# Performance work log

Measured on AMD Instinct MI355X. Metric: run time of the kernel, lower is better.

The kernel has to match this reference:

```python
import jax, jax.numpy as jnp
import numpy as np
import math

B, E, V, D, L = 2, 100000, 12500, 128, 4


def _ln(x, g, b, eps=1e-5):
    m = jnp.mean(x, axis=-1, keepdims=True)
    v = jnp.mean(jnp.square(x - m), axis=-1, keepdims=True)
    return (x - m) / jnp.sqrt(v + eps) * g + b


def setup_inputs() -> dict:
    key = jax.random.key(0)
    ks = jax.random.split(key, 20)
    s = 0.02
    inp = {
        "delta_noisy": jax.random.normal(ks[0], (B, E, 3), jnp.float32),
        "n": jax.random.randint(ks[1], (B,), 0, 1000, jnp.int32),
        "edge_index": jax.random.randint(ks[2], (2, E), 0, V, jnp.int32),
        "num_vertices": V,
        "w_in": jax.random.normal(ks[3], (3, D), jnp.float32) * s,
        "b_in": jnp.zeros((D,), jnp.float32),
        "W1": jax.random.normal(ks[4], (L, 2 * D, D), jnp.float32) * s,
        "b1": jnp.zeros((L, D), jnp.float32),
        "ln_g": jnp.ones((L, D), jnp.float32),
        "ln_b": jnp.zeros((L, D), jnp.float32),
        "W2": jax.random.normal(ks[5], (L, D, D), jnp.float32) * s,
        "b2": jnp.zeros((L, D), jnp.float32),
        "norm_g": jnp.ones((L, D), jnp.float32),
        "norm_b": jnp.zeros((L, D), jnp.float32),
        "te_w1": jax.random.normal(ks[6], (D, 4 * D), jnp.float32) * s,
        "te_b1": jnp.zeros((4 * D,), jnp.float32),
        "te_w2": jax.random.normal(ks[7], (4 * D, D), jnp.float32) * s,
        "te_b2": jnp.zeros((D,), jnp.float32),
        "w_out": jax.random.normal(ks[8], (D, 3), jnp.float32) * s,
        "b_out": jnp.zeros((3,), jnp.float32),
    }
    return inp


def reference(delta_noisy, n, edge_index, num_vertices, w_in, b_in, W1, b1,
              ln_g, ln_b, W2, b2, norm_g, norm_b, te_w1, te_b1, te_w2, te_b2,
              w_out, b_out):
    Bq, Eq, _ = delta_noisy.shape
    Dq = w_in.shape[1]
    src, dst = edge_index[0], edge_index[1]

    # input projection: (B,E,3) -> (B,E,D)
    h = delta_noisy @ w_in + b_in

    # sinusoidal timestep embedding + MLP
    half = Dq // 2
    freqs = jnp.exp(-math.log(10000.0) * jnp.arange(half, dtype=jnp.float32) / half)
    args = n.astype(jnp.float32)[:, None] * freqs[None, :]
    emb = jnp.concatenate([jnp.sin(args), jnp.cos(args)], axis=-1)  # (B,D)
    t_emb = jax.nn.silu(emb @ te_w1 + te_b1) @ te_w2 + te_b2
    h = h + t_emb[:, None, :]

    for i in range(W1.shape[0]):
        # scatter-add edge features into both endpoint vertices: (B,V,D)
        vf = jnp.zeros((Bq, num_vertices, Dq), h.dtype)
        vf = vf.at[:, src].add(h).at[:, dst].add(h)
        # gather back to edges and run edge MLP
        x = jnp.concatenate([vf[:, src, :], vf[:, dst, :]], axis=-1)  # (B,E,2D)
        x = x @ W1[i] + b1[i]
        x = jax.nn.silu(_ln(x, ln_g[i], ln_b[i]))
        x = x @ W2[i] + b2[i]
        h = _ln(h + x, norm_g[i], norm_b[i])

    return h @ w_out + b_out
```

## Files before the change

### kernel.cpp

```cpp
#include <hip/hip_runtime.h>
#include <math.h>

#define Bc 2
#define Ec 100000
#define Vc 12500
#define Dc 128
#define Lc 4

typedef __attribute__((ext_vector_type(4))) float f32x4;
typedef __attribute__((ext_vector_type(8))) short short8s;
typedef __attribute__((ext_vector_type(8))) __bf16 bf16x8;

static __device__ __forceinline__ short f2bf(float f) {
    unsigned u = __builtin_bit_cast(unsigned, f);
    unsigned r = (u + 0x7FFFu + ((u >> 16) & 1u)) >> 16;
    return (short)r;
}

static __device__ __forceinline__ float bf2f(short s) {
    unsigned u = ((unsigned)(unsigned short)s) << 16;
    return __builtin_bit_cast(float, u);
}

static __device__ __forceinline__ f32x4 mfma16(short8s a, short8s b, f32x4 c) {
    return __builtin_amdgcn_mfma_f32_16x16x32_bf16(
        __builtin_bit_cast(bf16x8, a), __builtin_bit_cast(bf16x8, b), c, 0, 0, 0);
}

#define SWZ(row, bytecol) ((((row) * 256) + (bytecol)) ^ (((row) & 7) << 4))

__global__ void t_emb_kernel(const int* __restrict__ n,
                             const float* __restrict__ te_w1, const float* __restrict__ te_b1,
                             const float* __restrict__ te_w2, const float* __restrict__ te_b2,
                             float* __restrict__ t_emb) {
    const int b = blockIdx.x;
    const int t = threadIdx.x;
    __shared__ float emb[Dc];
    __shared__ float hid[4 * Dc];
    const float nf = (float)n[b];
    const int half = Dc / 2;
    {
        int j = (t < half) ? t : (t - half);
        float freq = expf(-logf(10000.0f) * (float)j / (float)half);
        float arg = nf * freq;
        emb[t] = (t < half) ? sinf(arg) : cosf(arg);
    }
    __syncthreads();
    for (int jj = 0; jj < 4; ++jj) {
        int c = t + jj * Dc;
        float acc = te_b1[c];
        for (int k = 0; k < Dc; ++k) acc += emb[k] * te_w1[k * (4 * Dc) + c];
        hid[c] = acc / (1.0f + expf(-acc));
    }
    __syncthreads();
    float acc = te_b2[t];
    for (int k = 0; k < 4 * Dc; ++k) acc += hid[k] * te_w2[k * Dc + t];
    t_emb[b * Dc + t] = acc;
}

__global__ void input_proj_kernel(const float* __restrict__ delta,
                                  const float* __restrict__ w_in, const float* __restrict__ b_in,
                                  const float* __restrict__ t_emb,
                                  unsigned short* __restrict__ h) {
    int idx = blockIdx.x * blockDim.x + threadIdx.x;
    const int total = Bc * Ec * (Dc / 4);
    if (idx >= total) return;
    int dq = idx & (Dc / 4 - 1);
    int be = idx >> 5;
    int b = be / Ec;
    const float* dd = delta + (size_t)be * 3;
    float d0 = dd[0], d1 = dd[1], d2 = dd[2];
    float4 acc = ((const float4*)b_in)[dq];
    float4 te = ((const float4*)t_emb)[b * (Dc / 4) + dq];
    float4 w0 = ((const float4*)w_in)[dq];
    float4 w1 = ((const float4*)w_in)[(Dc / 4) + dq];
    float4 w2 = ((const float4*)w_in)[2 * (Dc / 4) + dq];
    acc.x += te.x + d0 * w0.x + d1 * w1.x + d2 * w2.x;
    acc.y += te.y + d0 * w0.y + d1 * w1.y + d2 * w2.y;
    acc.z += te.z + d0 * w0.z + d1 * w1.z + d2 * w2.z;
    acc.w += te.w + d0 * w0.w + d1 * w1.w + d2 * w2.w;
    short4 p;
    p.x = f2bf(acc.x); p.y = f2bf(acc.y); p.z = f2bf(acc.z); p.w = f2bf(acc.w);
    ((short4*)h)[idx] = p;
}

__global__ void convert_w_kernel(const float* __restrict__ W1, const float* __restrict__ W2,
                                 short* __restrict__ w1f, short* __restrict__ w2f) {
    int idx = blockIdx.x * blockDim.x + threadIdx.x;
    if (idx < Lc * 32768) {
        int l = idx >> 15;
        int j = idx & 7;
        int lane = (idx >> 3) & 63;
        int ks = (idx >> 9) & 7;
        int nt = (idx >> 12) & 7;
        int r = lane & 15, g = lane >> 4;
        int n = nt * 16 + r;
        int k = 32 * ks + 8 * g + j;
        w1f[idx] = f2bf(W1[((size_t)l * 256 + k) * 128 + n]);
    }
    if (idx < Lc * 16384) {
        int l = idx >> 14;
        int j = idx & 7;
        int lane = (idx >> 3) & 63;
        int ks = (idx >> 9) & 3;
        int nt = (idx >> 11) & 7;
        int r = lane & 15, g = lane >> 4;
        int n = nt * 16 + r;
        int k = 32 * ks + 8 * g + j;
        w2f[idx] = f2bf(W2[((size_t)l * 128 + k) * 128 + n]);
    }
}

__global__ void csr_zero_kernel(int* __restrict__ cnt) {
    int i = blockIdx.x * blockDim.x + threadIdx.x;
    if (i < Vc) cnt[i] = 0;
}

__global__ void csr_count_kernel(const int* __restrict__ src, const int* __restrict__ dst,
                                 int* __restrict__ cnt) {
    int i = blockIdx.x * blockDim.x + threadIdx.x;
    if (i >= 2 * Ec) return;
    int v = (i < Ec) ? src[i] : dst[i - Ec];
    atomicAdd(&cnt[v], 1);
}

__global__ void csr_scan_kernel(const int* __restrict__ cnt,
                                int* __restrict__ off, int* __restrict__ cur) {
    __shared__ int part[256];
    const int t = threadIdx.x;
    const int CH = (Vc + 255) / 256;
    int s = 0;
    for (int j = 0; j < CH; ++j) {
        int i = t * CH + j;
        if (i < Vc) s += cnt[i];
    }
    part[t] = s;
    __syncthreads();
    for (int ofs = 1; ofs < 256; ofs <<= 1) {
        int y = (t >= ofs) ? part[t - ofs] : 0;
        __syncthreads();
        part[t] += y;
        __syncthreads();
    }
    int run = part[t] - s;
    for (int j = 0; j < CH; ++j) {
        int i = t * CH + j;
        if (i < Vc) {
            off[i] = run;
            cur[i] = run;
            run += cnt[i];
        }
    }
    if (t == 255) off[Vc] = run;
}

__global__ void csr_fill_kernel(const int* __restrict__ src, const int* __restrict__ dst,
                                int* __restrict__ cur, int* __restrict__ adj) {
    int i = blockIdx.x * blockDim.x + threadIdx.x;
    if (i >= 2 * Ec) return;
    int e = (i < Ec) ? i : (i - Ec);
    int v = (i < Ec) ? src[e] : dst[e];
    int p = atomicAdd(&cur[v], 1);
    adj[p] = e;
}

__global__ void gather_kernel(const unsigned short* __restrict__ h,
                              const int* __restrict__ off, const int* __restrict__ adj,
                              short* __restrict__ vf) {
    int gw = blockIdx.x * 4 + (threadIdx.x >> 6);
    if (gw >= Bc * Vc) return;
    int b = (gw >= Vc) ? 1 : 0;
    int v = gw - b * Vc;
    int lane = threadIdx.x & 63;
    int o0 = off[v], o1 = off[v + 1];
    const short2* hb = (const short2*)(h + (size_t)b * Ec * Dc);
    float ax0 = 0.f, ay0 = 0.f, ax1 = 0.f, ay1 = 0.f;
    float ax2 = 0.f, ay2 = 0.f, ax3 = 0.f, ay3 = 0.f;
    int j = o0;
    for (; j + 4 <= o1; j += 4) {
        int e0 = adj[j], e1 = adj[j + 1], e2 = adj[j + 2], e3 = adj[j + 3];
        short2 x0 = hb[(size_t)e0 * 64 + lane];
        short2 x1 = hb[(size_t)e1 * 64 + lane];
        short2 x2 = hb[(size_t)e2 * 64 + lane];
        short2 x3 = hb[(size_t)e3 * 64 + lane];
        ax0 += bf2f(x0.x); ay0 += bf2f(x0.y);
        ax1 += bf2f(x1.x); ay1 += bf2f(x1.y);
        ax2 += bf2f(x2.x); ay2 += bf2f(x2.y);
        ax3 += bf2f(x3.x); ay3 += bf2f(x3.y);
    }
    for (; j < o1; ++j) {
        int e = adj[j];
        short2 x = hb[(size_t)e * 64 + lane];
        ax0 += bf2f(x.x); ay0 += bf2f(x.y);
    }
    float sx = (ax0 + ax1) + (ax2 + ax3);
    float sy = (ay0 + ay1) + (ay2 + ay3);
    short2 w;
    w.x = f2bf(sx);
    w.y = f2bf(sy);
    ((short2*)vf)[(size_t)gw * (Dc / 2) + lane] = w;
}

__launch_bounds__(64, 3)
__global__ void edge_layer_kernel(unsigned short* __restrict__ h,
                                  const short* __restrict__ vf,
                                  const int* __restrict__ src, const int* __restrict__ dst,
                                  const short* __restrict__ w1f, const float* __restrict__ b1,
                                  const float* __restrict__ ln_g, const float* __restrict__ ln_b,
                                  const short* __restrict__ w2f, const float* __restrict__ b2,
                                  const float* __restrict__ ng, const float* __restrict__ nb,
                                  const float* __restrict__ w_out, const float* __restrict__ b_out,
                                  float* __restrict__ out) {
    __shared__ __align__(16) short x1s[16 * 128];
    char* x1b = (char*)x1s;

    const int lane = threadIdx.x;
    const int r = lane & 15;
    const int g = lane >> 4;
    const int wavebase = blockIdx.x * 32;

    const short *srow[2], *drow[2];
    #pragma unroll
    for (int mt = 0; mt < 2; ++mt) {
        int eg = wavebase + mt * 16 + r;
        int bb = (eg >= Ec) ? 1 : 0;
        int e = eg - bb * Ec;
        srow[mt] = vf + ((size_t)(bb * Vc + src[e])) * Dc;
        drow[mt] = vf + ((size_t)(bb * Vc + dst[e])) * Dc;
    }

    short8s bf[2][8];
    #pragma unroll
    for (int mt = 0; mt < 2; ++mt)
        #pragma unroll
        for (int ks = 0; ks < 4; ++ks) {
            bf[mt][ks]     = *(const short8s*)(srow[mt] + 32 * ks + 8 * g);
            bf[mt][4 + ks] = *(const short8s*)(drow[mt] + 32 * ks + 8 * g);
        }

    f32x4 acc[2][8];
    #pragma unroll
    for (int nt = 0; nt < 8; ++nt) {
        acc[0][nt] = (f32x4){0.f, 0.f, 0.f, 0.f};
        acc[1][nt] = (f32x4){0.f, 0.f, 0.f, 0.f};
        #pragma unroll
        for (int ks = 0; ks < 8; ++ks) {
            short8s afrag = *(const short8s*)(w1f + ((size_t)(nt * 8 + ks) * 64 + lane) * 8);
            acc[0][nt] = mfma16(afrag, bf[0][ks], acc[0][nt]);
            acc[1][nt] = mfma16(afrag, bf[1][ks], acc[1][nt]);
        }
    }

    const bool last = (w_out != nullptr);

    #pragma unroll
    for (int mt = 0; mt < 2; ++mt) {
        const int eg = wavebase + mt * 16 + r;
        unsigned short* hrow = h + (size_t)eg * Dc;

        short4 hpre[8];
        #pragma unroll
        for (int nt = 0; nt < 8; ++nt)
            hpre[nt] = *(const short4*)(hrow + nt * 16 + 4 * g);

        {
            float s = 0.f, ss = 0.f;
            #pragma unroll
            for (int nt = 0; nt < 8; ++nt) {
                const float4 bb = *(const float4*)&b1[nt * 16 + 4 * g];
                acc[mt][nt][0] += bb.x; acc[mt][nt][1] += bb.y;
                acc[mt][nt][2] += bb.z; acc[mt][nt][3] += bb.w;
                #pragma unroll
                for (int i = 0; i < 4; ++i) { float v = acc[mt][nt][i]; s += v; ss += v * v; }
            }
            s += __shfl_xor(s, 16); ss += __shfl_xor(ss, 16);
            s += __shfl_xor(s, 32); ss += __shfl_xor(ss, 32);
            float mean = s * (1.0f / Dc);
            float var = ss * (1.0f / Dc) - mean * mean;
            float rstd = rsqrtf(var + 1e-5f);
            #pragma unroll
            for (int nt = 0; nt < 8; ++nt) {
                const float4 lg = *(const float4*)&ln_g[nt * 16 + 4 * g];
                const float4 lb = *(const float4*)&ln_b[nt * 16 + 4 * g];
                float o[4];
                #pragma unroll
                for (int i = 0; i < 4; ++i) {
                    float gg = (i == 0) ? lg.x : (i == 1) ? lg.y : (i == 2) ? lg.z : lg.w;
                    float bb = (i == 0) ? lb.x : (i == 1) ? lb.y : (i == 2) ? lb.z : lb.w;
                    float xh = (acc[mt][nt][i] - mean) * rstd * gg + bb;
                    o[i] = xh / (1.0f + __expf(-xh));
                }
                short4 st;
                st.x = f2bf(o[0]); st.y = f2bf(o[1]); st.z = f2bf(o[2]); st.w = f2bf(o[3]);
                *(short4*)(x1b + SWZ(r, (nt * 16 + 4 * g) * 2)) = st;
            }
        }

        short8s b2f[4];
        #pragma unroll
        for (int ks = 0; ks < 4; ++ks)
            b2f[ks] = *(const short8s*)(x1b + SWZ(r, (32 * ks + 8 * g) * 2));
        f32x4 acc2[8];
        #pragma unroll
        for (int nt = 0; nt < 8; ++nt) {
            acc2[nt] = (f32x4){0.f, 0.f, 0.f, 0.f};
            #pragma unroll
            for (int ks = 0; ks < 4; ++ks) {
                short8s afrag = *(const short8s*)(w2f + ((size_t)(nt * 4 + ks) * 64 + lane) * 8);
                acc2[nt] = mfma16(afrag, b2f[ks], acc2[nt]);
            }
        }

        float s = 0.f, ss = 0.f;
        #pragma unroll
        for (int nt = 0; nt < 8; ++nt) {
            const float4 bb = *(const float4*)&b2[nt * 16 + 4 * g];
            acc2[nt][0] += bb.x + bf2f(hpre[nt].x);
            acc2[nt][1] += bb.y + bf2f(hpre[nt].y);
            acc2[nt][2] += bb.z + bf2f(hpre[nt].z);
            acc2[nt][3] += bb.w + bf2f(hpre[nt].w);
            #pragma unroll
            for (int i = 0; i < 4; ++i) { float v = acc2[nt][i]; s += v; ss += v * v; }
        }
        s += __shfl_xor(s, 16); ss += __shfl_xor(ss, 16);
        s += __shfl_xor(s, 32); ss += __shfl_xor(ss, 32);
        float mean = s * (1.0f / Dc);
        float var = ss * (1.0f / Dc) - mean * mean;
        float rstd = rsqrtf(var + 1e-5f);
        if (!last) {
            #pragma unroll
            for (int nt = 0; nt < 8; ++nt) {
                const float4 gv = *(const float4*)&ng[nt * 16 + 4 * g];
                const float4 bv = *(const float4*)&nb[nt * 16 + 4 * g];
                short4 o;
                o.x = f2bf((acc2[nt][0] - mean) * rstd * gv.x + bv.x);
                o.y = f2bf((acc2[nt][1] - mean) * rstd * gv.y + bv.y);
                o.z = f2bf((acc2[nt][2] - mean) * rstd * gv.z + bv.z);
                o.w = f2bf((acc2[nt][3] - mean) * rstd * gv.w + bv.w);
                *(short4*)(hrow + nt * 16 + 4 * g) = o;
            }
        } else {
            float a0 = 0.f, a1 = 0.f, a2 = 0.f;
            #pragma unroll
            for (int nt = 0; nt < 8; ++nt) {
                const float4 gv = *(const float4*)&ng[nt * 16 + 4 * g];
                const float4 bv = *(const float4*)&nb[nt * 16 + 4 * g];
                #pragma unroll
                for (int i = 0; i < 4; ++i) {
                    float gg = (i == 0) ? gv.x : (i == 1) ? gv.y : (i == 2) ? gv.z : gv.w;
                    float bb = (i == 0) ? bv.x : (i == 1) ? bv.y : (i == 2) ? bv.z : bv.w;
                    float y = (acc2[nt][i] - mean) * rstd * gg + bb;
                    int nidx = nt * 16 + 4 * g + i;
                    a0 += y * w_out[nidx * 3 + 0];
                    a1 += y * w_out[nidx * 3 + 1];
                    a2 += y * w_out[nidx * 3 + 2];
                }
            }
            a0 += __shfl_xor(a0, 16); a1 += __shfl_xor(a1, 16); a2 += __shfl_xor(a2, 16);
            a0 += __shfl_xor(a0, 32); a1 += __shfl_xor(a1, 32); a2 += __shfl_xor(a2, 32);
            if (g == 0) {
                out[(size_t)eg * 3 + 0] = a0 + b_out[0];
                out[(size_t)eg * 3 + 1] = a1 + b_out[1];
                out[(size_t)eg * 3 + 2] = a2 + b_out[2];
            }
        }
    }
}

extern "C" void kernel_launch(void* const* d_in, const int* in_sizes, int n_in,
                              void* d_out, int out_size, void* d_ws, size_t ws_size,
                              hipStream_t stream) {
    const float* delta = (const float*)d_in[0];
    const int* n = (const int*)d_in[1];
    const int* edge_index = (const int*)d_in[2];
    const float* w_in = (const float*)d_in[4];
    const float* b_in = (const float*)d_in[5];
    const float* W1 = (const float*)d_in[6];
    const float* b1 = (const float*)d_in[7];
    const float* ln_g = (const float*)d_in[8];
    const float* ln_b = (const float*)d_in[9];
    const float* W2 = (const float*)d_in[10];
    const float* b2 = (const float*)d_in[11];
    const float* ng = (const float*)d_in[12];
    const float* nb = (const float*)d_in[13];
    const float* te_w1 = (const float*)d_in[14];
    const float* te_b1 = (const float*)d_in[15];
    const float* te_w2 = (const float*)d_in[16];
    const float* te_b2 = (const float*)d_in[17];
    const float* w_out = (const float*)d_in[18];
    const float* b_out = (const float*)d_in[19];
    float* out = (float*)d_out;

    char* ws = (char*)d_ws;
    size_t o = 0;
    float* t_emb = (float*)(ws + o); o += 1024;
    unsigned short* h = (unsigned short*)(ws + o); o += (size_t)Bc * Ec * Dc * 2;
    short* vf    = (short*)(ws + o); o += (size_t)Bc * Vc * Dc * 2;
    short* w1f   = (short*)(ws + o); o += (size_t)Lc * 32768 * 2;
    short* w2f   = (short*)(ws + o); o += (size_t)Lc * 16384 * 2;
    int* cnt     = (int*)(ws + o);   o += ((size_t)Vc * 4 + 255) / 256 * 256;
    int* off     = (int*)(ws + o);   o += ((size_t)(Vc + 1) * 4 + 255) / 256 * 256;
    int* cur     = (int*)(ws + o);   o += ((size_t)Vc * 4 + 255) / 256 * 256;
    int* adj     = (int*)(ws + o);   o += (size_t)2 * Ec * 4;

    const int* src = edge_index;
    const int* dst = edge_index + Ec;

    t_emb_kernel<<<Bc, Dc, 0, stream>>>(n, te_w1, te_b1, te_w2, te_b2, t_emb);
    convert_w_kernel<<<(Lc * 32768 + 255) / 256, 256, 0, stream>>>(W1, W2, w1f, w2f);

    {
        int total = Bc * Ec * (Dc / 4);
        input_proj_kernel<<<(total + 255) / 256, 256, 0, stream>>>(delta, w_in, b_in, t_emb, h);
    }

    csr_zero_kernel<<<(Vc + 255) / 256, 256, 0, stream>>>(cnt);
    csr_count_kernel<<<(2 * Ec + 255) / 256, 256, 0, stream>>>(src, dst, cnt);
    csr_scan_kernel<<<1, 256, 0, stream>>>(cnt, off, cur);
    csr_fill_kernel<<<(2 * Ec + 255) / 256, 256, 0, stream>>>(src, dst, cur, adj);

    const int eblocks = (Bc * Ec) / 32;
    for (int i = 0; i < Lc; ++i) {
        gather_kernel<<<(Bc * Vc + 3) / 4, 256, 0, stream>>>(h, off, adj, vf);
        edge_layer_kernel<<<eblocks, 64, 0, stream>>>(
            h, vf, src, dst,
            w1f + (size_t)i * 32768, b1 + i * Dc,
            ln_g + i * Dc, ln_b + i * Dc,
            w2f + (size_t)i * 16384, b2 + i * Dc,
            ng + i * Dc, nb + i * Dc,
            (i == Lc - 1) ? w_out : nullptr, b_out, out);
    }
}
```

Measured before the change: 688.2 us.

## Hoist first edge-MLP GEMM to per-vertex projections before gathering to edges

Splits W1 into its src and dst halves and applies each to the vertex features once per vertex in a new vertex_gemm_kernel, writing two bf16 projected tables. The edge kernel then gathers the two projected rows and adds them, skipping the 2D×D GEMM per edge. This cuts first-layer MFMA work by roughly the edge-to-vertex ratio. In exchange it adds a kernel launch, extra workspace and a write/read of two vertex-sized tables, plus an extra bf16 rounding of the projected values before the layer norm.

New measurement: 606.7 us. 1.13x faster.

```diff
diff --git a/kernel.cpp b/kernel.cpp
--- a/kernel.cpp
+++ b/kernel.cpp
@@ -26,8 +26,6 @@
     return __builtin_amdgcn_mfma_f32_16x16x32_bf16(
         __builtin_bit_cast(bf16x8, a), __builtin_bit_cast(bf16x8, b), c, 0, 0, 0);
 }
-
-#define SWZ(row, bytecol) ((((row) * 256) + (bytecol)) ^ (((row) & 7) << 4))
 
 __global__ void t_emb_kernel(const int* __restrict__ n,
                              const float* __restrict__ te_w1, const float* __restrict__ te_b1,
@@ -85,18 +83,19 @@
 }
 
 __global__ void convert_w_kernel(const float* __restrict__ W1, const float* __restrict__ W2,
-                                 short* __restrict__ w1f, short* __restrict__ w2f) {
+                                 short* __restrict__ w1af, short* __restrict__ w2f) {
     int idx = blockIdx.x * blockDim.x + threadIdx.x;
     if (idx < Lc * 32768) {
         int l = idx >> 15;
         int j = idx & 7;
         int lane = (idx >> 3) & 63;
-        int ks = (idx >> 9) & 7;
-        int nt = (idx >> 12) & 7;
+        int ks = (idx >> 9) & 3;
+        int nt = (idx >> 11) & 7;
+        int half = (idx >> 14) & 1;
         int r = lane & 15, g = lane >> 4;
         int n = nt * 16 + r;
-        int k = 32 * ks + 8 * g + j;
-        w1f[idx] = f2bf(W1[((size_t)l * 256 + k) * 128 + n]);
+        int k = half * 128 + 32 * ks + 8 * g + j;
+        w1af[idx] = f2bf(W1[((size_t)l * 256 + k) * 128 + n]);
     }
     if (idx < Lc * 16384) {
         int l = idx >> 14;
@@ -202,54 +201,94 @@
 }
 
 __launch_bounds__(64, 3)
+__global__ void vertex_gemm_kernel(const short* __restrict__ vf,
+                                   const short* __restrict__ w1af, const float* __restrict__ b1,
+                                   short* __restrict__ yA, short* __restrict__ yB) {
+    const int lane = threadIdx.x;
+    const int r = lane & 15;
+    const int g = lane >> 4;
+    const int vbase = blockIdx.x * 32;
+
+    int vv[2];
+    short8s bfrag[2][4];
+    #pragma unroll
+    for (int mt = 0; mt < 2; ++mt) {
+        int v = vbase + mt * 16 + r;
+        vv[mt] = v;
+        int vcl = (v < Bc * Vc) ? v : (Bc * Vc - 1);
+        const short* vrow = vf + (size_t)vcl * Dc;
+        #pragma unroll
+        for (int ks = 0; ks < 4; ++ks)
+            bfrag[mt][ks] = *(const short8s*)(vrow + 32 * ks + 8 * g);
+    }
+
+    #pragma unroll
+    for (int half = 0; half < 2; ++half) {
+        short* y = (half == 0) ? yA : yB;
+        f32x4 acc[2][8];
+        #pragma unroll
+        for (int nt = 0; nt < 8; ++nt) {
+            acc[0][nt] = (f32x4){0.f, 0.f, 0.f, 0.f};
+            acc[1][nt] = (f32x4){0.f, 0.f, 0.f, 0.f};
+            #pragma unroll
+            for (int ks = 0; ks < 4; ++ks) {
+                short8s afrag = *(const short8s*)(
+                    w1af + ((size_t)(((half * 8 + nt) * 4 + ks)) * 64 + lane) * 8);
+                acc[0][nt] = mfma16(afrag, bfrag[0][ks], acc[0][nt]);
+                acc[1][nt] = mfma16(afrag, bfrag[1][ks], acc[1][nt]);
+            }
+        }
+        #pragma unroll
+        for (int mt = 0; mt < 2; ++mt) {
+            if (vv[mt] >= Bc * Vc) continue;
+            short* yrow = y + (size_t)vv[mt] * Dc;
+            #pragma unroll
+            for (int nt = 0; nt < 8; ++nt) {
+                float4 bb = make_float4(0.f, 0.f, 0.f, 0.f);
+                if (half == 0) bb = *(const float4*)&b1[nt * 16 + 4 * g];
+                short4 st;
+                st.x = f2bf(acc[mt][nt][0] + bb.x);
+                st.y = f2bf(acc[mt][nt][1] + bb.y);
+                st.z = f2bf(acc[mt][nt][2] + bb.z);
+                st.w = f2bf(acc[mt][nt][3] + bb.w);
+                *(short4*)(yrow + nt * 16 + 4 * g) = st;
+            }
+        }
+    }
+}
+
+__launch_bounds__(64, 3)
 __global__ void edge_layer_kernel(unsigned short* __restrict__ h,
-                                  const short* __restrict__ vf,
+                                  const short* __restrict__ yA, const short* __restrict__ yB,
                                   const int* __restrict__ src, const int* __restrict__ dst,
-                                  const short* __restrict__ w1f, const float* __restrict__ b1,
                                   const float* __restrict__ ln_g, const float* __restrict__ ln_b,
                                   const short* __restrict__ w2f, const float* __restrict__ b2,
                                   const float* __restrict__ ng, const float* __restrict__ nb,
                                   const float* __restrict__ w_out, const float* __restrict__ b_out,
                                   float* __restrict__ out) {
-    __shared__ __align__(16) short x1s[16 * 128];
-    char* x1b = (char*)x1s;
-
     const int lane = threadIdx.x;
     const int r = lane & 15;
     const int g = lane >> 4;
     const int wavebase = blockIdx.x * 32;
 
-    const short *srow[2], *drow[2];
+    const short *arow[2], *brow[2];
     #pragma unroll
     for (int mt = 0; mt < 2; ++mt) {
         int eg = wavebase + mt * 16 + r;
         int bb = (eg >= Ec) ? 1 : 0;
         int e = eg - bb * Ec;
-        srow[mt] = vf + ((size_t)(bb * Vc + src[e])) * Dc;
-        drow[mt] = vf + ((size_t)(bb * Vc + dst[e])) * Dc;
-    }
-
-    short8s bf[2][8];
+        arow[mt] = yA + ((size_t)(bb * Vc + src[e])) * Dc;
+        brow[mt] = yB + ((size_t)(bb * Vc + dst[e])) * Dc;
+    }
+
+    short8s sa[2][4], sb[2][4];
     #pragma unroll
     for (int mt = 0; mt < 2; ++mt)
         #pragma unroll
         for (int ks = 0; ks < 4; ++ks) {
-            bf[mt][ks]     = *(const short8s*)(srow[mt] + 32 * ks + 8 * g);
-            bf[mt][4 + ks] = *(const short8s*)(drow[mt] + 32 * ks + 8 * g);
-        }
-
-    f32x4 acc[2][8];
-    #pragma unroll
-    for (int nt = 0; nt < 8; ++nt) {
-        acc[0][nt] = (f32x4){0.f, 0.f, 0.f, 0.f};
-        acc[1][nt] = (f32x4){0.f, 0.f, 0.f, 0.f};
-        #pragma unroll
-        for (int ks = 0; ks < 8; ++ks) {
-            short8s afrag = *(const short8s*)(w1f + ((size_t)(nt * 8 + ks) * 64 + lane) * 8);
-            acc[0][nt] = mfma16(afrag, bf[0][ks], acc[0][nt]);
-            acc[1][nt] = mfma16(afrag, bf[1][ks], acc[1][nt]);
-        }
-    }
+            sa[mt][ks] = *(const short8s*)(arow[mt] + 32 * ks + 8 * g);
+            sb[mt][ks] = *(const short8s*)(brow[mt] + 32 * ks + 8 * g);
+        }
 
     const bool last = (w_out != nullptr);
 
@@ -263,43 +302,41 @@
         for (int nt = 0; nt < 8; ++nt)
             hpre[nt] = *(const short4*)(hrow + nt * 16 + 4 * g);
 
-        {
-            float s = 0.f, ss = 0.f;
-            #pragma unroll
-            for (int nt = 0; nt < 8; ++nt) {
-                const float4 bb = *(const float4*)&b1[nt * 16 + 4 * g];
-                acc[mt][nt][0] += bb.x; acc[mt][nt][1] += bb.y;
-                acc[mt][nt][2] += bb.z; acc[mt][nt][3] += bb.w;
-                #pragma unroll
-                for (int i = 0; i < 4; ++i) { float v = acc[mt][nt][i]; s += v; ss += v * v; }
-            }
-            s += __shfl_xor(s, 16); ss += __shfl_xor(ss, 16);
-            s += __shfl_xor(s, 32); ss += __shfl_xor(ss, 32);
-            float mean = s * (1.0f / Dc);
-            float var = ss * (1.0f / Dc) - mean * mean;
-            float rstd = rsqrtf(var + 1e-5f);
-            #pragma unroll
-            for (int nt = 0; nt < 8; ++nt) {
-                const float4 lg = *(const float4*)&ln_g[nt * 16 + 4 * g];
-                const float4 lb = *(const float4*)&ln_b[nt * 16 + 4 * g];
-                float o[4];
-                #pragma unroll
-                for (int i = 0; i < 4; ++i) {
-                    float gg = (i == 0) ? lg.x : (i == 1) ? lg.y : (i == 2) ? lg.z : lg.w;
-                    float bb = (i == 0) ? lb.x : (i == 1) ? lb.y : (i == 2) ? lb.z : lb.w;
-                    float xh = (acc[mt][nt][i] - mean) * rstd * gg + bb;
-                    o[i] = xh / (1.0f + __expf(-xh));
-                }
-                short4 st;
-                st.x = f2bf(o[0]); st.y = f2bf(o[1]); st.z = f2bf(o[2]); st.w = f2bf(o[3]);
-                *(short4*)(x1b + SWZ(r, (nt * 16 + 4 * g) * 2)) = st;
-            }
-        }
-
-        short8s b2f[4];
+        float x1v[4][8];
+        float s = 0.f, ss = 0.f;
         #pragma unroll
         for (int ks = 0; ks < 4; ++ks)
-            b2f[ks] = *(const short8s*)(x1b + SWZ(r, (32 * ks + 8 * g) * 2));
+            #pragma unroll
+            for (int j = 0; j < 8; ++j) {
+                float v = bf2f(sa[mt][ks][j]) + bf2f(sb[mt][ks][j]);
+                x1v[ks][j] = v;
+                s += v; ss += v * v;
+            }
+        s += __shfl_xor(s, 16); ss += __shfl_xor(ss, 16);
+        s += __shfl_xor(s, 32); ss += __shfl_xor(ss, 32);
+        float mean = s * (1.0f / Dc);
+        float var = ss * (1.0f / Dc) - mean * mean;
+        float rstd = rsqrtf(var + 1e-5f);
+
+        short8s bfrag[4];
+        #pragma unroll
+        for (int ks = 0; ks < 4; ++ks) {
+            const float4 lg0 = *(const float4*)&ln_g[32 * ks + 8 * g];
+            const float4 lg1 = *(const float4*)&ln_g[32 * ks + 8 * g + 4];
+            const float4 lb0 = *(const float4*)&ln_b[32 * ks + 8 * g];
+            const float4 lb1 = *(const float4*)&ln_b[32 * ks + 8 * g + 4];
+            #pragma unroll
+            for (int j = 0; j < 8; ++j) {
+                float gg = (j < 4) ? ((j == 0) ? lg0.x : (j == 1) ? lg0.y : (j == 2) ? lg0.z : lg0.w)
+                                   : ((j == 4) ? lg1.x : (j == 5) ? lg1.y : (j == 6) ? lg1.z : lg1.w);
+                float bb = (j < 4) ? ((j == 0) ? lb0.x : (j == 1) ? lb0.y : (j == 2) ? lb0.z : lb0.w)
+                                   : ((j == 4) ? lb1.x : (j == 5) ? lb1.y : (j == 6) ? lb1.z : lb1.w);
+                float xh = (x1v[ks][j] - mean) * rstd * gg + bb;
+                float o = xh / (1.0f + __expf(-xh));
+                bfrag[ks][j] = f2bf(o);
+            }
+        }
+
         f32x4 acc2[8];
         #pragma unroll
         for (int nt = 0; nt < 8; ++nt) {
@@ -307,11 +344,11 @@
             #pragma unroll
             for (int ks = 0; ks < 4; ++ks) {
                 short8s afrag = *(const short8s*)(w2f + ((size_t)(nt * 4 + ks) * 64 + lane) * 8);
-                acc2[nt] = mfma16(afrag, b2f[ks], acc2[nt]);
-            }
-        }
-
-        float s = 0.f, ss = 0.f;
+                acc2[nt] = mfma16(afrag, bfrag[ks], acc2[nt]);
+            }
+        }
+
+        float s2 = 0.f, ss2 = 0.f;
         #pragma unroll
         for (int nt = 0; nt < 8; ++nt) {
             const float4 bb = *(const float4*)&b2[nt * 16 + 4 * g];
@@ -320,23 +357,23 @@
             acc2[nt][2] += bb.z + bf2f(hpre[nt].z);
             acc2[nt][3] += bb.w + bf2f(hpre[nt].w);
             #pragma unroll
-            for (int i = 0; i < 4; ++i) { float v = acc2[nt][i]; s += v; ss += v * v; }
-        }
-        s += __shfl_xor(s, 16); ss += __shfl_xor(ss, 16);
-        s += __shfl_xor(s, 32); ss += __shfl_xor(ss, 32);
-        float mean = s * (1.0f / Dc);
-        float var = ss * (1.0f / Dc) - mean * mean;
-        float rstd = rsqrtf(var + 1e-5f);
+            for (int i = 0; i < 4; ++i) { float v = acc2[nt][i]; s2 += v; ss2 += v * v; }
+        }
+        s2 += __shfl_xor(s2, 16); ss2 += __shfl_xor(ss2, 16);
+        s2 += __shfl_xor(s2, 32); ss2 += __shfl_xor(ss2, 32);
+        float mean2 = s2 * (1.0f / Dc);
+        float var2 = ss2 * (1.0f / Dc) - mean2 * mean2;
+        float rstd2 = rsqrtf(var2 + 1e-5f);
         if (!last) {
             #pragma unroll
             for (int nt = 0; nt < 8; ++nt) {
                 const float4 gv = *(const float4*)&ng[nt * 16 + 4 * g];
                 const float4 bv = *(const float4*)&nb[nt * 16 + 4 * g];
                 short4 o;
-                o.x = f2bf((acc2[nt][0] - mean) * rstd * gv.x + bv.x);
-                o.y = f2bf((acc2[nt][1] - mean) * rstd * gv.y + bv.y);
-                o.z = f2bf((acc2[nt][2] - mean) * rstd * gv.z + bv.z);
-                o.w = f2bf((acc2[nt][3] - mean) * rstd * gv.w + bv.w);
+                o.x = f2bf((acc2[nt][0] - mean2) * rstd2 * gv.x + bv.x);
+                o.y = f2bf((acc2[nt][1] - mean2) * rstd2 * gv.y + bv.y);
+                o.z = f2bf((acc2[nt][2] - mean2) * rstd2 * gv.z + bv.z);
+                o.w = f2bf((acc2[nt][3] - mean2) * rstd2 * gv.w + bv.w);
                 *(short4*)(hrow + nt * 16 + 4 * g) = o;
             }
         } else {
@@ -349,7 +386,7 @@
                 for (int i = 0; i < 4; ++i) {
                     float gg = (i == 0) ? gv.x : (i == 1) ? gv.y : (i == 2) ? gv.z : gv.w;
                     float bb = (i == 0) ? bv.x : (i == 1) ? bv.y : (i == 2) ? bv.z : bv.w;
-                    float y = (acc2[nt][i] - mean) * rstd * gg + bb;
+                    float y = (acc2[nt][i] - mean2) * rstd2 * gg + bb;
                     int nidx = nt * 16 + 4 * g + i;
                     a0 += y * w_out[nidx * 3 + 0];
                     a1 += y * w_out[nidx * 3 + 1];
@@ -396,7 +433,9 @@
     float* t_emb = (float*)(ws + o); o += 1024;
     unsigned short* h = (unsigned short*)(ws + o); o += (size_t)Bc * Ec * Dc * 2;
     short* vf    = (short*)(ws + o); o += (size_t)Bc * Vc * Dc * 2;
-    short* w1f   = (short*)(ws + o); o += (size_t)Lc * 32768 * 2;
+    short* yA    = (short*)(ws + o); o += (size_t)Bc * Vc * Dc * 2;
+    short* yB    = (short*)(ws + o); o += (size_t)Bc * Vc * Dc * 2;
+    short* w1af  = (short*)(ws + o); o += (size_t)Lc * 32768 * 2;
     short* w2f   = (short*)(ws + o); o += (size_t)Lc * 16384 * 2;
     int* cnt     = (int*)(ws + o);   o += ((size_t)Vc * 4 + 255) / 256 * 256;
     int* off     = (int*)(ws + o);   o += ((size_t)(Vc + 1) * 4 + 255) / 256 * 256;
@@ -407,7 +446,7 @@
     const int* dst = edge_index + Ec;
 
     t_emb_kernel<<<Bc, Dc, 0, stream>>>(n, te_w1, te_b1, te_w2, te_b2, t_emb);
-    convert_w_kernel<<<(Lc * 32768 + 255) / 256, 256, 0, stream>>>(W1, W2, w1f, w2f);
+    convert_w_kernel<<<(Lc * 32768 + 255) / 256, 256, 0, stream>>>(W1, W2, w1af, w2f);
 
     {
         int total = Bc * Ec * (Dc / 4);
@@ -419,12 +458,14 @@
     csr_scan_kernel<<<1, 256, 0, stream>>>(cnt, off, cur);
     csr_fill_kernel<<<(2 * Ec + 255) / 256, 256, 0, stream>>>(src, dst, cur, adj);
 
+    const int vblocks = (Bc * Vc + 31) / 32;
     const int eblocks = (Bc * Ec) / 32;
     for (int i = 0; i < Lc; ++i) {
         gather_kernel<<<(Bc * Vc + 3) / 4, 256, 0, stream>>>(h, off, adj, vf);
+        vertex_gemm_kernel<<<vblocks, 64, 0, stream>>>(
+            vf, w1af + (size_t)i * 32768, b1 + i * Dc, yA, yB);
         edge_layer_kernel<<<eblocks, 64, 0, stream>>>(
-            h, vf, src, dst,
-            w1f + (size_t)i * 32768, b1 + i * Dc,
+            h, yA, yB, src, dst,
             ln_g + i * Dc, ln_b + i * Dc,
             w2f + (size_t)i * 16384, b2 + i * Dc,
             ng + i * Dc, nb + i * Dc,
```
